# Performance work log

Measured on AMD Instinct MI355X. Metric: run time of the kernel, lower is better.

The kernel has to match this reference:

```python
import jax, jax.numpy as jnp
import numpy as np
from jax import lax

DIM = 256
NUM_HEADS = 8
HEAD_DIM = DIM // NUM_HEADS
SCALE = HEAD_DIM ** -0.5


def _avg_pool(x, k, p):
    # torch AvgPool2d(kernel=k, stride=1, padding=p) with count_include_pad=True
    s = lax.reduce_window(x, 0.0, lax.add,
                          window_dimensions=(1, 1, k, k),
                          window_strides=(1, 1, 1, 1),
                          padding=((0, 0), (0, 0), (p, p), (p, p)))
    return s / (k * k)


def setup_inputs() -> dict:
    key = jax.random.key(0)
    ks = jax.random.split(key, 7)
    x = jax.random.normal(ks[0], (2, DIM, 48, 48), dtype=jnp.float32)
    q_w = jax.random.normal(ks[1], (DIM, DIM), dtype=jnp.float32) * (DIM ** -0.5)
    q_b = jax.random.normal(ks[2], (DIM,), dtype=jnp.float32) * 0.02
    kv_w = jax.random.normal(ks[3], (2 * DIM, DIM), dtype=jnp.float32) * (DIM ** -0.5)
    kv_b = jax.random.normal(ks[4], (2 * DIM,), dtype=jnp.float32) * 0.02
    proj_w = jax.random.normal(ks[5], (DIM, DIM), dtype=jnp.float32) * (DIM ** -0.5)
    proj_b = jax.random.normal(ks[6], (DIM,), dtype=jnp.float32) * 0.02
    return {"x": x, "q_w": q_w, "q_b": q_b, "kv_w": kv_w, "kv_b": kv_b,
            "proj_w": proj_w, "proj_b": proj_b}


def reference(x, q_w, q_b, kv_w, kv_b, proj_w, proj_b):
    B, C, H, W = x.shape
    h, d, N = NUM_HEADS, HEAD_DIM, H * W

    # q = 1x1 conv -> [B, h, N, d]
    q = jnp.einsum('oc,bchw->bohw', q_w, x) + q_b[None, :, None, None]
    q = q.reshape(B, h, d, N).transpose(0, 1, 3, 2)

    # kv is a linear 1x1 conv, so (kv(x)+kv(p1)+kv(p2)+kv(p3))/4 == kv(mean of inputs)
    x_avg = (x + _avg_pool(x, 3, 1) + _avg_pool(x, 5, 2) + _avg_pool(x, 7, 3)) / 4.0
    kv = jnp.einsum('oc,bchw->bohw', kv_w, x_avg) + kv_b[None, :, None, None]
    kv = kv.reshape(B, 2, h, d, N).transpose(1, 0, 2, 4, 3)  # [2, B, h, N, d]
    k, v = kv[0], kv[1]

    attn = jnp.einsum('bhnd,bhmd->bhnm', q, k) * SCALE  # [B, h, N, N]
    attn = jax.nn.softmax(attn, axis=-1)
    y = jnp.einsum('bhnm,bhmd->bhnd', attn, v)  # [B, h, N, d]
    # faithful to torch: transpose(1,2) then flat reshape to [B, C, H, W]
    y = y.transpose(0, 2, 1, 3).reshape(B, C, H, W)

    out = jnp.einsum('oc,bchw->bohw', proj_w, y) + proj_b[None, :, None, None]
    return out
```

## Files before the change

kernel.cpp:

```cpp
#include <hip/hip_runtime.h>
#include <hip/hip_bf16.h>
#include <cstdint>

#define DIMC  256
#define NH    8
#define HD    32
#define NPIX  2304
#define BATCH 2
#define KT    32
#define NTW   18
#define KPW   576

typedef short s16x8 __attribute__((ext_vector_type(8)));
typedef short s16x4 __attribute__((ext_vector_type(4)));
typedef float f32x4 __attribute__((ext_vector_type(4)));

#define MFMA32(A,B,C) __builtin_amdgcn_mfma_f32_16x16x32_bf16(A,B,C,0,0,0)

__device__ inline uint32_t rnau(float x) { return __float_as_uint(x) + 0x8000u; }
__device__ inline uint32_t pk2(uint32_t l_, uint32_t h_) {
  return __builtin_amdgcn_perm(h_, l_, 0x07060302u);
}

__global__ __launch_bounds__(256) void pool_kernel(const float* __restrict__ x,
                                                   float* __restrict__ xavg) {
  const int plane = blockIdx.x;
  const float* xp = x + (size_t)plane * NPIX;
  __shared__ float sx[NPIX];
  __shared__ float h3[NPIX], h5[NPIX], h7[NPIX];
  const int t = threadIdx.x;
#pragma unroll
  for (int r = 0; r < 9; ++r) sx[r * 256 + t] = xp[r * 256 + t];
  __syncthreads();
#pragma unroll
  for (int r = 0; r < 9; ++r) {
    int p = r * 256 + t;
    int i = p / 48, j = p - i * 48;
    float a3 = 0.f, a5 = 0.f, a7 = 0.f;
#pragma unroll
    for (int dj = -3; dj <= 3; ++dj) {
      int jj = j + dj;
      if (jj < 0 || jj >= 48) continue;
      float v = sx[i * 48 + jj];
      a7 += v;
      if (dj >= -2 && dj <= 2) a5 += v;
      if (dj >= -1 && dj <= 1) a3 += v;
    }
    h3[p] = a3; h5[p] = a5; h7[p] = a7;
  }
  __syncthreads();
#pragma unroll
  for (int r = 0; r < 9; ++r) {
    int p = r * 256 + t;
    int i = p / 48, j = p - i * 48;
    float b3 = 0.f, b5 = 0.f, b7 = 0.f;
#pragma unroll
    for (int di = -3; di <= 3; ++di) {
      int ii = i + di;
      if (ii < 0 || ii >= 48) continue;
      int q = ii * 48 + j;
      b7 += h7[q];
      if (di >= -2 && di <= 2) b5 += h5[q];
      if (di >= -1 && di <= 1) b3 += h3[q];
    }
    xavg[(size_t)plane * NPIX + p] =
        0.25f * (sx[p] + b3 * (1.f / 9.f) + b5 * (1.f / 25.f) + b7 * (1.f / 49.f));
  }
}

__global__ __launch_bounds__(256) void conv_all(
    const float* __restrict__ x, const float* __restrict__ xavg,
    const float* __restrict__ qw, const float* __restrict__ kvw,
    const float* __restrict__ pw_,
    short* __restrict__ Xh, short* __restrict__ Ah,
    short* __restrict__ Wth) {
  const int bx = blockIdx.x;
  const int t = threadIdx.x;
  if (bx < 576) {
    const float* src = (bx < 288) ? x : xavg;
    short* dhi = (bx < 288) ? Xh : Ah;
    const int bb = (bx < 288) ? bx : bx - 288;
    const int n0 = (bb % 36) * 64, c0 = ((bb / 36) & 3) * 64, b = bb / 144;
    __shared__ __align__(16) float T[64][68];
    {
      const int c = t >> 2, n4 = (t & 3) * 16;
      const float* sp = src + ((size_t)b * DIMC + c0 + c) * NPIX + n0 + n4;
#pragma unroll
      for (int i2 = 0; i2 < 4; ++i2)
        *(f32x4*)&T[c][n4 + i2 * 4] = *(const f32x4*)(sp + i2 * 4);
    }
    __syncthreads();
    {
      const int n = t >> 2, c4 = (t & 3) * 16;
      float v[16];
#pragma unroll
      for (int i = 0; i < 16; ++i) v[i] = T[c4 + i][n];
      uint32_t a[16];
#pragma unroll
      for (int i = 0; i < 16; ++i) a[i] = rnau(v[i]);
      union { s16x8 s; uint32_t u[4]; } H0, H1;
#pragma unroll
      for (int j = 0; j < 4; ++j) {
        H0.u[j] = pk2(a[2 * j], a[2 * j + 1]);
        H1.u[j] = pk2(a[8 + 2 * j], a[8 + 2 * j + 1]);
      }
      const size_t off = ((size_t)b * NPIX + n0 + n) * DIMC + c0 + c4;
      *(s16x8*)(dhi + off) = H0.s; *(s16x8*)(dhi + off + 8) = H1.s;
    }
  } else {
    const int idx = ((bx - 576) * 256 + t) * 8;
    const float* s;
    int off;
    if (idx < 65536)       { s = qw;  off = idx; }
    else if (idx < 196608) { s = kvw; off = idx - 65536; }
    else                   { s = pw_; off = idx - 196608; }
    f32x4 x0 = *(const f32x4*)(s + off);
    f32x4 x1 = *(const f32x4*)(s + off + 4);
    float v[8] = {x0[0], x0[1], x0[2], x0[3], x1[0], x1[1], x1[2], x1[3]};
    uint32_t a[8];
#pragma unroll
    for (int i = 0; i < 8; ++i) a[i] = rnau(v[i]);
    union { s16x8 s; uint32_t u[4]; } H;
#pragma unroll
    for (int j = 0; j < 4; ++j) H.u[j] = pk2(a[2 * j], a[2 * j + 1]);
    *(s16x8*)(Wth + idx) = H.s;
  }
}

__global__ __launch_bounds__(128) void gemm_qkv_hi(
    const short* __restrict__ Wth,
    const float* __restrict__ q_b, const float* __restrict__ kv_b,
    const short* __restrict__ Xh, const short* __restrict__ Ah,
    short* __restrict__ Qhi, short* __restrict__ Khi, short* __restrict__ Vhi,
    float qscale) {
  __shared__ __align__(16) float Cl[32][68];
  const int by = blockIdx.y;
  const bool isQ = (by < 8);
  const int o0 = isQ ? by * 32 : (by - 8) * 32;
  const short* Wh = isQ ? Wth : Wth + 65536;
  const float* bias = isQ ? q_b : kv_b;
  const short* Inh = isQ ? Xh : Ah;
  const float scale = isQ ? qscale : 1.0f;
  short* d1 = isQ ? Qhi : Khi;
  const int n0 = blockIdx.x * 64;
  const int b  = blockIdx.z;

  const int tid = threadIdx.x;
  const int wave = tid >> 6, lane = tid & 63;
  const int g = lane >> 4, q = lane & 15;

  const short* wph = Wh + ((o0 + wave * 16 + q) * DIMC + g * 8);
  const short* iph = Inh + ((size_t)(b * NPIX + n0 + q) * DIMC + g * 8);

  f32x4 acc[4] = {{0,0,0,0},{0,0,0,0},{0,0,0,0},{0,0,0,0}};
#pragma unroll
  for (int c0 = 0; c0 < DIMC; c0 += 32) {
    s16x8 ah = *(const s16x8*)(wph + c0);
#pragma unroll
    for (int st = 0; st < 4; ++st) {
      s16x8 bh_ = *(const s16x8*)(iph + (size_t)st * 16 * DIMC + c0);
      acc[st] = MFMA32(ah, bh_, acc[st]);
    }
  }
#pragma unroll
  for (int st = 0; st < 4; ++st)
#pragma unroll
    for (int r = 0; r < 4; ++r)
      Cl[wave * 16 + g * 4 + r][st * 16 + q] = acc[st][r];
  __syncthreads();

  if (o0 < 256) {
    const int n = tid >> 1, oq = tid & 1;
    const int h = o0 >> 5;
    const float* bp = bias + o0 + oq * 16;
    float v[16];
#pragma unroll
    for (int i = 0; i < 16; ++i) v[i] = (Cl[oq * 16 + i][n] + bp[i]) * scale;
    uint32_t a[16];
#pragma unroll
    for (int i = 0; i < 16; ++i) a[i] = rnau(v[i]);
    union { s16x8 s; uint32_t u[4]; } H0, H1;
#pragma unroll
    for (int j = 0; j < 4; ++j) {
      H0.u[j] = pk2(a[2 * j], a[2 * j + 1]);
      H1.u[j] = pk2(a[8 + 2 * j], a[8 + 2 * j + 1]);
    }
    const size_t off = ((size_t)((b * 8 + h) * NPIX + n0 + n)) * HD + oq * 16;
    *(s16x8*)(d1 + off) = H0.s; *(s16x8*)(d1 + off + 8) = H1.s;
  } else {
    const int o = tid >> 2, nc = (tid & 3) * 16;
    const int h = (o0 - 256) >> 5;
    const float bv = bias[o0 + o];
    float v[16];
#pragma unroll
    for (int i2 = 0; i2 < 4; ++i2) {
      f32x4 t4 = *(const f32x4*)&Cl[o][nc + i2 * 4];
      v[i2 * 4 + 0] = t4[0] + bv; v[i2 * 4 + 1] = t4[1] + bv;
      v[i2 * 4 + 2] = t4[2] + bv; v[i2 * 4 + 3] = t4[3] + bv;
    }
    uint32_t a[16];
#pragma unroll
    for (int i = 0; i < 16; ++i) a[i] = rnau(v[i]);
    union { s16x8 s; uint32_t u[4]; } H0, H1;
#pragma unroll
    for (int j = 0; j < 4; ++j) {
      H0.u[j] = pk2(a[2 * j], a[2 * j + 1]);
      H1.u[j] = pk2(a[8 + 2 * j], a[8 + 2 * j + 1]);
    }
    const size_t off = ((size_t)((b * 8 + h) * HD + o)) * NPIX + n0 + nc;
    *(s16x8*)(Vhi + off) = H0.s; *(s16x8*)(Vhi + off + 8) = H1.s;
  }
}

__global__ __launch_bounds__(256) void attn_fused(
    const short* __restrict__ Qhi,
    const short* __restrict__ Khi,
    const short* __restrict__ Vhi,
    short* __restrict__ zh) {
  const int blk = blockIdx.x;
  const int bh = blk / 72;
  const int qb = blk % 72;
  const int tid = threadIdx.x;
  const int wave = tid >> 6, lane = tid & 63;
  const int g = lane >> 4, q = lane & 15;
  const int base = qb * 32;

  __shared__ __align__(16) float smemf[4 * 64 * 20];
  short* pwA = (short*)smemf + wave * 1280;
  short* pwB = pwA + 640;
  float (*R)[64][20] = (float (*)[64][20])smemf;

  const size_t qoff = ((size_t)bh * NPIX + base + q) * HD + g * 8;
  const s16x8 qhA = *(const s16x8*)(Qhi + qoff);
  const s16x8 qhB = *(const s16x8*)(Qhi + qoff + 16 * HD);

  const short* kp = Khi + ((size_t)bh * NPIX + wave * KPW + q) * HD + g * 8;
  const short* vp = Vhi + ((size_t)bh * HD + q) * NPIX + wave * KPW + g * 8;

  const f32x4 Z4 = {0.f, 0.f, 0.f, 0.f};
  f32x4 OA0 = Z4, OA1 = Z4, OB0 = Z4, OB1 = Z4;
  f32x4 LA = Z4, LB = Z4;
  s16x8 kb[3][2], vb[3][2], pfA, pfB, vp0, vp1;

  union { s16x8 s; uint32_t u[4]; } ONE, ZZ;
  ONE.u[0] = 0x3F803F80u; ONE.u[1] = 0x3F803F80u;
  ONE.u[2] = 0x3F803F80u; ONE.u[3] = 0x3F803F80u;
  ZZ.u[0] = 0; ZZ.u[1] = 0; ZZ.u[2] = 0; ZZ.u[3] = 0;
  const s16x8 ones = ONE.s;
  pfA = ZZ.s; pfB = ZZ.s;
  vp0 = ones; vp1 = ones;

  kb[0][0] = *(const s16x8*)(kp);
  kb[0][1] = *(const s16x8*)(kp + 16 * HD);
  vb[0][0] = *(const s16x8*)(vp);
  vb[0][1] = *(const s16x8*)(vp + 16 * NPIX);
  kb[1][0] = *(const s16x8*)(kp + KT * HD);
  kb[1][1] = *(const s16x8*)(kp + KT * HD + 16 * HD);
  vb[1][0] = *(const s16x8*)(vp + KT);
  vb[1][1] = *(const s16x8*)(vp + KT + 16 * NPIX);

#define ATTN_STEP(CUR, NX2, T)                                                \
  {                                                                           \
    if ((T) + 2 < NTW) {                                                      \
      const short* kpn = kp + ((T) + 2) * (KT * HD);                          \
      const short* vpn = vp + ((T) + 2) * KT;                                 \
      kb[NX2][0] = *(const s16x8*)(kpn);                                      \
      kb[NX2][1] = *(const s16x8*)(kpn + 16 * HD);                            \
      vb[NX2][0] = *(const s16x8*)(vpn);                                      \
      vb[NX2][1] = *(const s16x8*)(vpn + 16 * NPIX);                          \
    }                                                                         \
    f32x4 SA0 = MFMA32(kb[CUR][0], qhA, Z4);                                  \
    f32x4 SA1 = MFMA32(kb[CUR][1], qhA, Z4);                                  \
    f32x4 SB0 = MFMA32(kb[CUR][0], qhB, Z4);                                  \
    f32x4 SB1 = MFMA32(kb[CUR][1], qhB, Z4);                                  \
    OA0 = MFMA32(vp0, pfA, OA0);                                              \
    OA1 = MFMA32(vp1, pfA, OA1);                                              \
    OB0 = MFMA32(vp0, pfB, OB0);                                              \
    OB1 = MFMA32(vp1, pfB, OB1);                                              \
    LA  = MFMA32(ones, pfA, LA);                                              \
    LB  = MFMA32(ones, pfB, LB);                                              \
    {                                                                         \
      f32x4 p0, p1;                                                           \
      p0[0] = exp2f(SA0[0]); p0[1] = exp2f(SA0[1]);                           \
      p0[2] = exp2f(SA0[2]); p0[3] = exp2f(SA0[3]);                           \
      p1[0] = exp2f(SA1[0]); p1[1] = exp2f(SA1[1]);                           \
      p1[2] = exp2f(SA1[2]); p1[3] = exp2f(SA1[3]);                           \
      uint2 w0, w1;                                                           \
      w0.x = pk2(rnau(p0[0]), rnau(p0[1])); w0.y = pk2(rnau(p0[2]), rnau(p0[3])); \
      w1.x = pk2(rnau(p1[0]), rnau(p1[1])); w1.y = pk2(rnau(p1[2]), rnau(p1[3])); \
      *(uint2*)&pwA[q * 40 + g * 4] = w0;                                     \
      *(uint2*)&pwA[q * 40 + 16 + g * 4] = w1;                                \
    }                                                                         \
    {                                                                         \
      f32x4 p0, p1;                                                           \
      p0[0] = exp2f(SB0[0]); p0[1] = exp2f(SB0[1]);                           \
      p0[2] = exp2f(SB0[2]); p0[3] = exp2f(SB0[3]);                           \
      p1[0] = exp2f(SB1[0]); p1[1] = exp2f(SB1[1]);                           \
      p1[2] = exp2f(SB1[2]); p1[3] = exp2f(SB1[3]);                           \
      uint2 w0, w1;                                                           \
      w0.x = pk2(rnau(p0[0]), rnau(p0[1])); w0.y = pk2(rnau(p0[2]), rnau(p0[3])); \
      w1.x = pk2(rnau(p1[0]), rnau(p1[1])); w1.y = pk2(rnau(p1[2]), rnau(p1[3])); \
      *(uint2*)&pwB[q * 40 + g * 4] = w0;                                     \
      *(uint2*)&pwB[q * 40 + 16 + g * 4] = w1;                                \
    }                                                                         \
    vp0 = vb[CUR][0]; vp1 = vb[CUR][1];                                       \
    pfA = *(const s16x8*)&pwA[q * 40 + g * 8];                                \
    pfB = *(const s16x8*)&pwB[q * 40 + g * 8];                                \
  }

#pragma unroll 1
  for (int tt = 0; tt < NTW; tt += 3) {
    ATTN_STEP(0, 2, tt);
    ATTN_STEP(1, 0, tt + 1);
    ATTN_STEP(2, 1, tt + 2);
  }
#undef ATTN_STEP

  OA0 = MFMA32(vp0, pfA, OA0);
  OA1 = MFMA32(vp1, pfA, OA1);
  OB0 = MFMA32(vp0, pfB, OB0);
  OB1 = MFMA32(vp1, pfB, OB1);
  LA  = MFMA32(ones, pfA, LA);
  LB  = MFMA32(ones, pfB, LB);

  __syncthreads();
  {
    float* rw = &R[wave][lane][0];
    *(f32x4*)&rw[0]  = OA0;
    *(f32x4*)&rw[4]  = OA1;
    *(f32x4*)&rw[8]  = OB0;
    *(f32x4*)&rw[12] = OB1;
    rw[16] = LA[0];
    rw[17] = LB[0];
  }
  __syncthreads();
  {
    const int l2 = tid & 63, eg = tid >> 6;
    const int g2 = l2 >> 4, q2 = l2 & 15;
    f32x4 s = {0.f, 0.f, 0.f, 0.f};
    float Lt = 0.f;
#pragma unroll
    for (int w = 0; w < 4; ++w) {
      const f32x4 pv = *(const f32x4*)&R[w][l2][eg * 4];
      s[0] += pv[0]; s[1] += pv[1]; s[2] += pv[2]; s[3] += pv[3];
      Lt += R[w][l2][16 + (eg >> 1)];
    }
    const float inv = 1.f / Lt;
    const int h = bh & 7, b = bh >> 3;
    const int n = base + ((eg & 2) ? 16 : 0) + q2;
    const int d0 = ((eg & 1) ? 16 : 0) + g2 * 4;
    const int c = n / 9, r = n - c * 9;
    short* zp = zh + ((size_t)(b * NPIX + r * 256 + h * HD + d0)) * DIMC + c;
#pragma unroll
    for (int j = 0; j < 4; ++j)
      zp[(size_t)j * DIMC] = (short)(rnau(s[j] * inv) >> 16);
  }
}

__global__ __launch_bounds__(128) void gemm_proj_hi(
    const short* __restrict__ Wh,
    const float* __restrict__ bias,
    const short* __restrict__ Zh,
    float* __restrict__ out) {
  __shared__ __align__(16) float Cl[32][68];
  const int n0 = blockIdx.x * 64;
  const int o0 = blockIdx.y * 32;
  const int b  = blockIdx.z;
  const int tid = threadIdx.x;
  const int wave = tid >> 6, lane = tid & 63;
  const int g = lane >> 4, q = lane & 15;

  const short* wph = Wh + ((o0 + wave * 16 + q) * DIMC + g * 8);
  const short* iph = Zh + ((size_t)(b * NPIX + n0 + q) * DIMC + g * 8);

  f32x4 acc[4] = {{0,0,0,0},{0,0,0,0},{0,0,0,0},{0,0,0,0}};
#pragma unroll
  for (int c0 = 0; c0 < DIMC; c0 += 32) {
    s16x8 ah = *(const s16x8*)(wph + c0);
#pragma unroll
    for (int st = 0; st < 4; ++st) {
      s16x8 bh_ = *(const s16x8*)(iph + (size_t)st * 16 * DIMC + c0);
      acc[st] = MFMA32(ah, bh_, acc[st]);
    }
  }
#pragma unroll
  for (int st = 0; st < 4; ++st)
#pragma unroll
    for (int r = 0; r < 4; ++r)
      Cl[wave * 16 + g * 4 + r][st * 16 + q] = acc[st][r];
  __syncthreads();

  const int o = tid >> 2, nc = (tid & 3) * 16;
  const float bv = bias[o0 + o];
  float* op = out + ((size_t)b * DIMC + o0 + o) * NPIX + n0 + nc;
#pragma unroll
  for (int i2 = 0; i2 < 4; ++i2) {
    f32x4 v = *(const f32x4*)&Cl[o][nc + i2 * 4];
    v[0] += bv; v[1] += bv; v[2] += bv; v[3] += bv;
    *(f32x4*)(op + i2 * 4) = v;
  }
}

extern "C" void kernel_launch(void* const* d_in, const int* in_sizes, int n_in,
                              void* d_out, int out_size, void* d_ws, size_t ws_size,
                              hipStream_t stream) {
  const float* x      = (const float*)d_in[0];
  const float* q_w    = (const float*)d_in[1];
  const float* q_b    = (const float*)d_in[2];
  const float* kv_w   = (const float*)d_in[3];
  const float* kv_b   = (const float*)d_in[4];
  const float* proj_w = (const float*)d_in[5];
  const float* proj_b = (const float*)d_in[6];
  float* out = (float*)d_out;

  char* w = (char*)d_ws;
  float* xavg = (float*)w;
  short* Xh   = (short*)(w + 4718592);
  short* Ah   = (short*)(w + 9437184);
  short* Wth  = (short*)(w + 28311552);
  short* Qhi  = (short*)(w + 29360128);
  short* Khi  = (short*)(w + 31719424);
  short* Vhi  = (short*)(w + 34078720);
  short* Zh   = (short*)(w + 37322752);

  const float qscale = 0.17677669529663689f * 1.4426950408889634f;

  pool_kernel<<<BATCH * DIMC, 256, 0, stream>>>(x, xavg);
  conv_all<<<704, 256, 0, stream>>>(x, xavg, q_w, kv_w, proj_w, Xh, Ah, Wth);
  gemm_qkv_hi<<<dim3(36, 24, 2), 128, 0, stream>>>(Wth, q_b, kv_b,
                                                   Xh, Ah, Qhi, Khi, Vhi, qscale);
  attn_fused<<<1152, 256, 0, stream>>>(Qhi, Khi, Vhi, Zh);
  gemm_proj_hi<<<dim3(36, 8, 2), 128, 0, stream>>>(Wth + 196608, proj_b, Zh, out);
}
```

Before: 147.9 us.

## Split attention keys across eight waves and remap block-to-head order

The attention kernel now launches 512 threads per block, with eight waves each handling 288 keys instead of four waves handling 576, which halves each wave's serial key loop. The cross-wave reduction is rewritten so each thread sums two outputs over eight partials. Block indices are also interleaved across heads, likely for better cache or XCD locality of K/V. The cost is twice as much shared memory for the reduction and more reduction work per block, and the new launch bounds may limit registers per thread.

Result: slower. 275.6 us (+86.3%).

```diff
diff --git a/kernel.cpp b/kernel.cpp
--- a/kernel.cpp
+++ b/kernel.cpp
@@ -8,8 +8,9 @@
 #define NPIX  2304
 #define BATCH 2
 #define KT    32
-#define NTW   18
-#define KPW   576
+#define NWAVE 8
+#define NTW   9
+#define KPW   288
 
 typedef short s16x8 __attribute__((ext_vector_type(8)));
 typedef short s16x4 __attribute__((ext_vector_type(4)));
@@ -212,20 +213,21 @@
   }
 }
 
-__global__ __launch_bounds__(256) void attn_fused(
+__global__ __launch_bounds__(512, 6) void attn_fused(
     const short* __restrict__ Qhi,
     const short* __restrict__ Khi,
     const short* __restrict__ Vhi,
     short* __restrict__ zh) {
-  const int blk = blockIdx.x;
-  const int bh = blk / 72;
-  const int qb = blk % 72;
+  const int li = blockIdx.x;
+  const int r144 = li >> 3;
+  const int bh = 2 * (li & 7) + (r144 >= 72 ? 1 : 0);
+  const int qb = (r144 >= 72) ? r144 - 72 : r144;
   const int tid = threadIdx.x;
   const int wave = tid >> 6, lane = tid & 63;
   const int g = lane >> 4, q = lane & 15;
   const int base = qb * 32;
 
-  __shared__ __align__(16) float smemf[4 * 64 * 20];
+  __shared__ __align__(16) float smemf[8 * 64 * 20];
   short* pwA = (short*)smemf + wave * 1280;
   short* pwB = pwA + 640;
   float (*R)[64][20] = (float (*)[64][20])smemf;
@@ -337,23 +339,24 @@
   {
     const int l2 = tid & 63, eg = tid >> 6;
     const int g2 = l2 >> 4, q2 = l2 & 15;
-    f32x4 s = {0.f, 0.f, 0.f, 0.f};
-    float Lt = 0.f;
-#pragma unroll
-    for (int w = 0; w < 4; ++w) {
-      const f32x4 pv = *(const f32x4*)&R[w][l2][eg * 4];
-      s[0] += pv[0]; s[1] += pv[1]; s[2] += pv[2]; s[3] += pv[3];
-      Lt += R[w][l2][16 + (eg >> 1)];
+    const int isB = eg >> 2;
+    const int idx = (eg & 3) * 2;
+    float s0 = 0.f, s1 = 0.f, Lt = 0.f;
+#pragma unroll
+    for (int w = 0; w < NWAVE; ++w) {
+      const float* rw = &R[w][l2][0];
+      s0 += rw[isB * 8 + idx];
+      s1 += rw[isB * 8 + idx + 1];
+      Lt += rw[16 + isB];
     }
     const float inv = 1.f / Lt;
     const int h = bh & 7, b = bh >> 3;
-    const int n = base + ((eg & 2) ? 16 : 0) + q2;
-    const int d0 = ((eg & 1) ? 16 : 0) + g2 * 4;
+    const int n = base + isB * 16 + q2;
+    const int d0 = (idx < 4) ? (g2 * 4 + idx) : (16 + g2 * 4 + (idx - 4));
     const int c = n / 9, r = n - c * 9;
     short* zp = zh + ((size_t)(b * NPIX + r * 256 + h * HD + d0)) * DIMC + c;
-#pragma unroll
-    for (int j = 0; j < 4; ++j)
-      zp[(size_t)j * DIMC] = (short)(rnau(s[j] * inv) >> 16);
+    zp[0]    = (short)(rnau(s0 * inv) >> 16);
+    zp[DIMC] = (short)(rnau(s1 * inv) >> 16);
   }
 }
 
@@ -429,6 +432,6 @@
   conv_all<<<704, 256, 0, stream>>>(x, xavg, q_w, kv_w, proj_w, Xh, Ah, Wth);
   gemm_qkv_hi<<<dim3(36, 24, 2), 128, 0, stream>>>(Wth, q_b, kv_b,
                                                    Xh, Ah, Qhi, Khi, Vhi, qscale);
-  attn_fused<<<1152, 256, 0, stream>>>(Qhi, Khi, Vhi, Zh);
+  attn_fused<<<1152, 512, 0, stream>>>(Qhi, Khi, Vhi, Zh);
   gemm_proj_hi<<<dim3(36, 8, 2), 128, 0, stream>>>(Wth + 196608, proj_b, Zh, out);
 }
```
